# Kernel optimization log

Hardware: AMD Instinct MI355X
Metric: run time of the kernel (lower is better)

The kernel has to match this reference:

```python
import jax, jax.numpy as jnp
import numpy as np

PI = 3.1415927410125732
N = 4096
L = 1.28e-3          # box side [m]
VEL = 5e-7
RC = 3.15e-6         # Rc = diameter/2
RR = 8e-6
RO = 2.5e-5
RA = np.inf
DT_TRANS = 1.4e-14   # DT (translational diffusion)
DR = 0.0028
GAMMA = 25.0
DT = 0.2             # timestep dt
COLL_ITERS = 30      # fixed cap for collision-resolution do-while (orig caps at 1000)


def setup_inputs() -> dict:
    key = jax.random.key(0)
    ks = jax.random.split(key, 7)
    pos_re = jax.random.uniform(ks[0], (N,), jnp.float32) * L
    pos_im = jax.random.uniform(ks[1], (N,), jnp.float32) * L
    ang = jax.random.uniform(ks[2], (N,), jnp.float32, -PI, PI)
    ori_re = jnp.cos(ang)
    ori_im = jnp.sin(ang)
    deltas = jax.random.uniform(ks[3], (N,), jnp.float32) * 0.5
    rot_noise = jax.random.normal(ks[4], (N,), jnp.float32)
    tn_re = jax.random.normal(ks[5], (N,), jnp.float32)
    tn_im = jax.random.normal(ks[6], (N,), jnp.float32)
    return {"pos_re": pos_re, "pos_im": pos_im, "ori_re": ori_re, "ori_im": ori_im,
            "deltas": deltas, "rot_noise": rot_noise, "tn_re": tn_re, "tn_im": tn_im}


def _wrap(diff):
    # torch get_anglediff wrap: (-2pi,2pi) -> ~(-pi,pi)
    diff = jnp.where(diff <= -PI, jnp.mod(diff, PI), diff)
    return diff - (diff >= PI).astype(diff.dtype) * (2.0 * PI)


def _anglediff(a, b):
    return _wrap(jnp.angle(a) - jnp.angle(b))


def _cossim(a, b):
    # nn.CosineSimilarity(dim=1, eps=1e-14) on view_as_real vectors
    dot = a.real * b.real + a.imag * b.imag
    na = jnp.maximum(jnp.abs(a), 1e-14)
    nb = jnp.maximum(jnp.abs(b), 1e-14)
    return dot / (na * nb)


def _mvc(W, z):
    # real [n,n] mask @ complex [n] vector
    return W @ z.real + 1j * (W @ z.imag)


def _solve_collisions(pos):
    n = pos.shape[0]
    eye_f = jnp.eye(n, dtype=jnp.float32)
    eye_c = eye_f.astype(pos.dtype)

    def step(p):
        diff = p[None, :] - p[:, None] + eye_c  # [i,j] = pos_j - pos_i; diag dummy 1 (nan-safe)
        absd = jnp.abs(diff)
        coll = absd <= (2.0 * RC - eye_f)       # diag threshold negative -> self excluded
        move = jnp.where(coll, diff / jnp.where(coll, absd, 1.0) * ((2.1 * RC - absd) * 0.5), 0.0)
        return p - move.sum(axis=1), coll.sum()

    def body(carry, _):
        p, cont = carry
        p_new, ncoll = step(p)
        p = jnp.where(cont, p_new, p)           # do-while: apply move, then continue if collisions
        return (p, jnp.logical_and(cont, ncoll > 0)), None

    body = jax.checkpoint(body)
    (pos, _), _ = jax.lax.scan(body, (pos, jnp.array(True)), None, length=COLL_ITERS)
    return pos


def _forward(pos_re, pos_im, ori_re, ori_im, deltas, rot_noise, tn_re, tn_im):
    pos = (pos_re + 1j * pos_im).astype(jnp.complex64)
    ori = (ori_re + 1j * ori_im).astype(jnp.complex64)
    n = pos.shape[0]
    eye_b = jnp.eye(n, dtype=bool)

    # pairwise |pos_i - pos_j|; diag made 1 to keep abs() grad-safe (diag is masked out / re-added below)
    dists = jnp.abs(pos[:, None] - pos[None, :] + jnp.eye(n, dtype=pos.dtype))
    mask_rr = (dists <= RR) & ~eye_b              # repulsion zone, self excluded (eye subtracted in orig)
    mask_ro = (dists <= RO + RC) | eye_b          # orientation zone, self included (diag dist 0 in orig)
    mask_ra = (dists <= RA + RC) | eye_b          # Ra = inf -> all ones

    # alpha == 2*pi exactly -> within_view branch skipped (matches original)
    ang = jnp.angle(ori)
    abs_ad = jnp.abs(_wrap(ang[:, None] - ang[None, :]))
    in_front = abs_ad < PI / 2

    Wrr = (mask_rr & in_front).astype(jnp.float32)
    Wro = mask_ro.astype(jnp.float32)
    Wra = mask_ra.astype(jnp.float32)

    n_r = Wrr.sum(axis=1)
    S = _mvc(Wrr, pos) / jnp.maximum(n_r, 1.0) - pos * jnp.sign(n_r)
    d = -S

    n_a = Wra.sum(axis=1)
    cms = _mvc(Wra, pos) / jnp.maximum(n_a, 1.0)
    Ps = cms - pos * jnp.sign(n_a)

    osum = _mvc(Wro, ori)
    left = Ps * jnp.exp(1j * deltas)
    right = Ps * jnp.exp(-1j * deltas)

    # T (=300) >= T_release (=200): choose best turn by cosine similarity
    best = jnp.where(_cossim(left, osum) >= _cossim(right, osum), left, right)

    has_rep = jnp.abs(d) > 0.0
    d_safe = jnp.where(has_rep, d, jnp.ones_like(d))
    att = jnp.where(has_rep, _anglediff(d_safe, ori), _anglediff(best, ori))

    s2dr = np.float32(np.sqrt(2.0 * DR))
    sdt = np.float32(np.sqrt(DT))
    rot = jnp.exp(1j * (DT * GAMMA * DR * jnp.sin(att) + rot_noise * s2dr * sdt))

    # complex standard normal: real/imag each N(0, 1/sqrt(2))
    tnoise = (tn_re + 1j * tn_im) * np.float32(np.sqrt(0.5)) * np.float32(np.sqrt(2.0 * DT_TRANS))
    trans = DT * VEL * ori + tnoise * sdt

    new_pos = _solve_collisions(pos + trans)
    new_ori = ori * rot

    c2r = lambda z: jnp.stack([z.real, z.imag], axis=-1)
    # [5, N, 2]: positions, orientations, orientation_sums, leftturns, rightturns (real views)
    return jnp.stack([c2r(new_pos), c2r(new_ori), c2r(osum), c2r(left), c2r(right)], axis=0)


def reference(pos_re, pos_im, ori_re, ori_im, deltas, rot_noise, tn_re, tn_im):
    return _forward(pos_re, pos_im, ori_re, ori_im, deltas, rot_noise, tn_re, tn_im)
```

## Files before the change

kernel.cpp:

```cpp
#include <hip/hip_runtime.h>

#define NPART 4096
#define PI_F 3.1415927410125732f
#define TWO_PI_F 6.2831854820251465f
#define NBCAP 14336
#define SENT 4096

__device__ __forceinline__ float wrapf(float d) {
    if (d <= -PI_F) {
        d = fmodf(d, PI_F);
        if (d < 0.0f) d += PI_F;
    }
    if (d >= PI_F) d -= TWO_PI_F;
    return d;
}

__global__ __launch_bounds__(512)
void k_interact(const float* __restrict__ pr, const float* __restrict__ pim,
                const float* __restrict__ orr, const float* __restrict__ oim,
                const float* __restrict__ deltas,
                const float* __restrict__ rot_noise,
                const float* __restrict__ tn_re, const float* __restrict__ tn_im,
                float* __restrict__ out,
                float2* __restrict__ recPos, int* __restrict__ recMeta,
                unsigned short* __restrict__ recNbr, int* __restrict__ gcnt) {
    constexpr float RR_F  = 8e-6f;
    constexpr float RR2   = RR_F * RR_F;
    constexpr float ROC_F = (float)(2.5e-5 + 3.15e-6);
    constexpr float ROC2  = ROC_F * ROC_F;
    constexpr float CUT_F = 14.3e-6f;
    constexpr float CUT2  = CUT_F * CUT_F;

    __shared__ float2 lsP[512];
    __shared__ float2 lsO[512];
    __shared__ float rA0[512], rA1[512], rA2[512], rA3[512], rA4[512];
    __shared__ float rB0[512], rB1[512], rB2[512], rB3[512], rB4[512];
    __shared__ float cr_[512], ci_[512];
    __shared__ int ncnt[16];
    __shared__ unsigned short nbrL[16 * 16];

    int tid = threadIdx.x;
    int li = tid & 7, sl = tid >> 3;
    int i0 = blockIdx.x * 16 + li;
    int i1 = i0 + 8;

    if (tid < 16) ncnt[tid] = 0;

    float pxA = pr[i0], pyA = pim[i0], oxA = orr[i0], oyA = oim[i0];
    float pxB = pr[i1], pyB = pim[i1], oxB = orr[i1], oyB = oim[i1];

    float nAr = 0.0f, SAre = 0.0f, SAim = 0.0f, oAre = 0.0f, oAim = 0.0f;
    float nBr = 0.0f, SBre = 0.0f, SBim = 0.0f, oBre = 0.0f, oBim = 0.0f;
    float cs_re = 0.0f, cs_im = 0.0f;

    for (int c = 0; c < 8; ++c) {
        int j0 = c * 512;
        __syncthreads();
        float jr = pr[j0 + tid], ji = pim[j0 + tid];
        lsP[tid] = make_float2(jr, ji);
        lsO[tid] = make_float2(orr[j0 + tid], oim[j0 + tid]);
        cs_re += jr; cs_im += ji;
        __syncthreads();
#pragma unroll
        for (int t = 0; t < 8; ++t) {
            int jj = sl * 8 + ((t + sl) & 7);
            int j = j0 + jj;
            float2 pv = lsP[jj];
            float drA = pxA - pv.x, diA = pyA - pv.y;
            float d2A = drA * drA + diA * diA;
            float drB = pxB - pv.x, diB = pyB - pv.y;
            float d2B = drB * drB + diB * diB;
            if (__any((d2A <= ROC2) | (d2B <= ROC2))) {
                float2 ov = lsO[jj];
                if (d2A <= ROC2) { oAre += ov.x; oAim += ov.y; }
                float dotA = oxA * ov.x + oyA * ov.y;
                if ((d2A <= RR2) & (dotA > 0.0f) & (j != i0)) {
                    nAr += 1.0f; SAre += pv.x; SAim += pv.y;
                }
                if (d2A <= CUT2 && j != i0) {
                    int slot = atomicAdd(&ncnt[li], 1);
                    if (slot < 16) nbrL[li * 16 + slot] = (unsigned short)j;
                }
                if (d2B <= ROC2) { oBre += ov.x; oBim += ov.y; }
                float dotB = oxB * ov.x + oyB * ov.y;
                if ((d2B <= RR2) & (dotB > 0.0f) & (j != i1)) {
                    nBr += 1.0f; SBre += pv.x; SBim += pv.y;
                }
                if (d2B <= CUT2 && j != i1) {
                    int slot = atomicAdd(&ncnt[li + 8], 1);
                    if (slot < 16) nbrL[(li + 8) * 16 + slot] = (unsigned short)j;
                }
            }
        }
    }

    rA0[tid] = nAr; rA1[tid] = SAre; rA2[tid] = SAim; rA3[tid] = oAre; rA4[tid] = oAim;
    rB0[tid] = nBr; rB1[tid] = SBre; rB2[tid] = SBim; rB3[tid] = oBre; rB4[tid] = oBim;
    cr_[tid] = cs_re; ci_[tid] = cs_im;
    __syncthreads();
    for (int s = 256; s >= 8; s >>= 1) {
        if (tid < s) {
            rA0[tid] += rA0[tid + s]; rA1[tid] += rA1[tid + s];
            rA2[tid] += rA2[tid + s]; rA3[tid] += rA3[tid + s];
            rA4[tid] += rA4[tid + s];
            rB0[tid] += rB0[tid + s]; rB1[tid] += rB1[tid + s];
            rB2[tid] += rB2[tid + s]; rB3[tid] += rB3[tid + s];
            rB4[tid] += rB4[tid + s];
            cr_[tid] += cr_[tid + s];  ci_[tid] += ci_[tid + s];
        }
        __syncthreads();
    }
    if (tid < 4) { cr_[tid] += cr_[tid + 4]; ci_[tid] += ci_[tid + 4]; }
    __syncthreads();
    if (tid < 2) { cr_[tid] += cr_[tid + 2]; ci_[tid] += ci_[tid + 2]; }
    __syncthreads();
    if (tid == 0) { cr_[0] += cr_[1]; ci_[0] += ci_[1]; }
    __syncthreads();

    if (tid < 16) {
        int i = blockIdx.x * 16 + tid;
        float n_r, S_re, S_im, o_re, o_im, px, py, ox, oy;
        if (tid < 8) {
            n_r = rA0[tid]; S_re = rA1[tid]; S_im = rA2[tid];
            o_re = rA3[tid]; o_im = rA4[tid];
            px = pxA; py = pyA; ox = oxA; oy = oyA;
        } else {
            int g = tid - 8;
            n_r = rB0[g]; S_re = rB1[g]; S_im = rB2[g];
            o_re = rB3[g]; o_im = rB4[g];
            px = pxB; py = pyB; ox = oxB; oy = oyB;
        }

        float maxnr = fmaxf(n_r, 1.0f);
        float sgn = (n_r > 0.0f) ? 1.0f : 0.0f;
        float Sre = S_re / maxnr - px * sgn;
        float Sim = S_im / maxnr - py * sgn;
        float d_re = -Sre, d_im = -Sim;

        float cmsx = cr_[0] * (1.0f / 4096.0f);
        float cmsy = ci_[0] * (1.0f / 4096.0f);
        float Ps_re = cmsx - px;
        float Ps_im = cmsy - py;

        float dl = deltas[i];
        float cd = cosf(dl), sd = sinf(dl);
        float l_re = Ps_re * cd - Ps_im * sd;
        float l_im = Ps_re * sd + Ps_im * cd;
        float r_re = Ps_re * cd + Ps_im * sd;
        float r_im = Ps_im * cd - Ps_re * sd;

        float nb   = fmaxf(hypotf(o_re, o_im), 1e-14f);
        float na_l = fmaxf(hypotf(l_re, l_im), 1e-14f);
        float na_r = fmaxf(hypotf(r_re, r_im), 1e-14f);
        float csl = (l_re * o_re + l_im * o_im) / (na_l * nb);
        float csr = (r_re * o_re + r_im * o_im) / (na_r * nb);
        float b_re = (csl >= csr) ? l_re : r_re;
        float b_im = (csl >= csr) ? l_im : r_im;

        float ai = atan2f(oy, ox);
        bool has_rep = (d_re != 0.0f) || (d_im != 0.0f);
        float att;
        if (has_rep) att = wrapf(atan2f(d_im, d_re) - ai);
        else         att = wrapf(atan2f(b_im, b_re) - ai);

        constexpr float GDD  = (float)(0.2 * 25.0 * 0.0028);
        constexpr float S2DR = 0.07483314773547883f;
        constexpr float SDT  = 0.44721359549995793f;
        float theta = GDD * sinf(att) + (rot_noise[i] * S2DR) * SDT;
        float rr_ = cosf(theta), ri_ = sinf(theta);

        float no_re = ox * rr_ - oy * ri_;
        float no_im = ox * ri_ + oy * rr_;

        constexpr float DTVEL = (float)(0.2 * 5e-7);
        constexpr float C1 = 0.70710678118654752f;
        constexpr float C2 = 1.6733200530681511e-07f;
        float t_re = DTVEL * ox + ((tn_re[i] * C1) * C2) * SDT;
        float t_im = DTVEL * oy + ((tn_im[i] * C1) * C2) * SDT;
        float p0x = px + t_re, p0y = py + t_im;

        float2* o2 = (float2*)out;
        o2[i]            = make_float2(p0x, p0y);
        o2[1 * 4096 + i] = make_float2(no_re, no_im);
        o2[2 * 4096 + i] = make_float2(o_re, o_im);
        o2[3 * 4096 + i] = make_float2(l_re, l_im);
        o2[4 * 4096 + i] = make_float2(r_re, r_im);

        int c = min(ncnt[tid], 16);
        if (c > 0) {
            int cp = (c + 3) & ~3;
            int slot = atomicAdd(&gcnt[0], 1);
            int eoff = atomicAdd(&gcnt[1], cp);
            if (eoff + cp <= NBCAP) {
                recPos[slot] = make_float2(p0x, p0y);
                recMeta[slot] = i | (c << 12) | (eoff << 17);
                for (int m = 0; m < cp; ++m)
                    recNbr[eoff + m] = (m < c) ? nbrL[tid * 16 + m]
                                               : (unsigned short)SENT;
            } else {
                recPos[slot] = make_float2(p0x, p0y);
                recMeta[slot] = i;
            }
        }
    }
}

__global__ __launch_bounds__(1024)
void k_coll_all(const float2* __restrict__ recPos, const int* __restrict__ recMeta,
                const unsigned short* __restrict__ recNbr,
                const int* __restrict__ gcnt, float* __restrict__ out) {
    constexpr float TWO_RC  = (float)(2.0 * 3.15e-6);
    constexpr float TWO_RC2 = TWO_RC * TWO_RC;
    constexpr float C21RC   = (float)(2.1 * 3.15e-6);

    __shared__ float2 pos[NPART + 2];
    __shared__ unsigned short stamp[NPART + 2];
    __shared__ int flg[2];

    int tid = threadIdx.x;
    int n = gcnt[0];

    for (int k = tid; k < NPART + 2; k += 1024) stamp[k] = 0xFFFFu;
    if (tid == 0) {
        pos[SENT] = make_float2(1e9f, 1e9f);
        flg[0] = 0; flg[1] = 0;
    }

    float myx[4], myy[4];
    int myi[4], myc[4], myo[4];
    int nq0[4], nq1[4], nq2[4], nq3[4];
    bool mvd[4];
#pragma unroll
    for (int s = 0; s < 4; ++s) {
        int slot = s * 1024 + tid;
        myc[s] = 0; myi[s] = SENT; myo[s] = 0;
        nq0[s] = SENT; nq1[s] = SENT; nq2[s] = SENT; nq3[s] = SENT;
        mvd[s] = false;
        if (slot < n) {
            float2 p = recPos[slot];
            int meta = recMeta[slot];
            myx[s] = p.x; myy[s] = p.y;
            myi[s] = meta & 4095;
            myc[s] = (meta >> 12) & 31;
            myo[s] = (unsigned)meta >> 17;
            pos[myi[s]] = p;
            if (myc[s] > 0) {
                uint2 w = *(const uint2*)&recNbr[myo[s]];
                nq0[s] = w.x & 0xffff; nq1[s] = w.x >> 16;
                nq2[s] = w.y & 0xffff; nq3[s] = w.y >> 16;
            }
        }
    }
    __syncthreads();

    const float2 FARP = make_float2(1e9f, 1e9f);
    for (int it = 0; it < 30; ++it) {
        float nx[4], ny[4];
        int ncs[4];
#pragma unroll
        for (int s = 0; s < 4; ++s) {
            ncs[s] = 0;
            int c = myc[s];
            if (c <= 0) continue;
            bool chk = (it == 0) || mvd[s];
            if (!chk) {
                unsigned last = (unsigned)(it - 1);
                chk = (stamp[nq0[s]] == last);
                if (c > 1) chk |= (stamp[nq1[s]] == last);
                if (c > 2) chk |= (stamp[nq2[s]] == last);
                if (c > 3) chk |= (stamp[nq3[s]] == last);
                for (int m0 = 4; m0 < c && !chk; m0 += 4) {
                    uint2 w = *(const uint2*)&recNbr[myo[s] + m0];
                    chk |= (stamp[w.x & 0xffff] == last);
                    if (m0 + 1 < c) chk |= (stamp[w.x >> 16] == last);
                    if (m0 + 2 < c) chk |= (stamp[w.y & 0xffff] == last);
                    if (m0 + 3 < c) chk |= (stamp[w.y >> 16] == last);
                }
            }
            if (!chk) continue;
            float px = myx[s], py = myy[s];
            float mre = 0.0f, mim = 0.0f;
            int nc = 0;
            float2 q0 = pos[nq0[s]];
            float2 q1 = (c > 1) ? pos[nq1[s]] : FARP;
            float2 q2 = (c > 2) ? pos[nq2[s]] : FARP;
            float2 q3 = (c > 3) ? pos[nq3[s]] : FARP;
#define COLL_ONE(q)                                                     \
            {                                                           \
                float dr = (q).x - px, di = (q).y - py;                 \
                float d2 = dr * dr + di * di;                           \
                if (d2 <= TWO_RC2) {                                    \
                    float a = sqrtf(d2);                                \
                    float mm = (C21RC - a) * 0.5f / a;                  \
                    mre += dr * mm; mim += di * mm; ++nc;               \
                }                                                       \
            }
            COLL_ONE(q0) COLL_ONE(q1) COLL_ONE(q2) COLL_ONE(q3)
            for (int m0 = 4; m0 < c; m0 += 4) {
                uint2 w = *(const uint2*)&recNbr[myo[s] + m0];
                int j0 = w.x & 0xffff, j1 = w.x >> 16;
                int j2 = w.y & 0xffff, j3 = w.y >> 16;
                float2 t0 = pos[j0], t1 = pos[j1], t2 = pos[j2], t3 = pos[j3];
                COLL_ONE(t0) COLL_ONE(t1) COLL_ONE(t2) COLL_ONE(t3)
            }
#undef COLL_ONE
            ncs[s] = nc;
            nx[s] = px - mre; ny[s] = py - mim;
        }
        __syncthreads();
        int any = 0;
#pragma unroll
        for (int s = 0; s < 4; ++s) {
            mvd[s] = (ncs[s] > 0);
            if (ncs[s] > 0) {
                myx[s] = nx[s]; myy[s] = ny[s];
                pos[myi[s]] = make_float2(nx[s], ny[s]);
                stamp[myi[s]] = (unsigned short)it;
                any = 1;
            }
        }
        if (any) flg[it & 1] = 1;
        if (tid == 0) flg[(it + 1) & 1] = 0;
        __syncthreads();
        if (flg[it & 1] == 0) break;
    }

    float2* o2 = (float2*)out;
#pragma unroll
    for (int s = 0; s < 4; ++s)
        if (s * 1024 + tid < n) o2[myi[s]] = make_float2(myx[s], myy[s]);
}

extern "C" void kernel_launch(void* const* d_in, const int* in_sizes, int n_in,
                              void* d_out, int out_size, void* d_ws, size_t ws_size,
                              hipStream_t stream) {
    const float* pos_re = (const float*)d_in[0];
    const float* pos_im = (const float*)d_in[1];
    const float* ori_re = (const float*)d_in[2];
    const float* ori_im = (const float*)d_in[3];
    const float* deltas = (const float*)d_in[4];
    const float* rot_noise = (const float*)d_in[5];
    const float* tn_re = (const float*)d_in[6];
    const float* tn_im = (const float*)d_in[7];
    float* out = (float*)d_out;

    int* gcnt = (int*)d_ws;
    float2* recPos = (float2*)((char*)d_ws + 16);
    int* recMeta   = (int*)(recPos + NPART);
    unsigned short* recNbr = (unsigned short*)(recMeta + NPART);

    hipMemsetAsync(gcnt, 0, 16, stream);
    k_interact<<<256, 512, 0, stream>>>(pos_re, pos_im, ori_re, ori_im,
                                        deltas, rot_noise, tn_re, tn_im,
                                        out, recPos, recMeta, recNbr, gcnt);
    k_coll_all<<<1, 1024, 0, stream>>>(recPos, recMeta, recNbr, gcnt, out);
}
```

Baseline: 124.2 us.

## Use fixed-slot neighbor lists and push-style dirty flags in collision solver

Replaces the atomic-compacted record list with a fixed 16-slot neighbor array indexed directly by particle id, which removes the global atomics and the memset launch. The collision kernel now reads positions back from the output buffer. The per-iteration activity check becomes push-based: a particle that moved stamps all its neighbors, so the pull-side check is a single flag lookup instead of a scan over neighbor stamps. In exchange, writes scatter into shared flags, which relies on neighbor lists being symmetric, and there are more idle threads because each particle keeps a fixed slot.

Measured after the change: 117.5 us. 5.4% less time.

```diff
diff --git a/kernel.cpp b/kernel.cpp
--- a/kernel.cpp
+++ b/kernel.cpp
@@ -3,7 +3,6 @@
 #define NPART 4096
 #define PI_F 3.1415927410125732f
 #define TWO_PI_F 6.2831854820251465f
-#define NBCAP 14336
 #define SENT 4096
 
 __device__ __forceinline__ float wrapf(float d) {
@@ -22,8 +21,7 @@
                 const float* __restrict__ rot_noise,
                 const float* __restrict__ tn_re, const float* __restrict__ tn_im,
                 float* __restrict__ out,
-                float2* __restrict__ recPos, int* __restrict__ recMeta,
-                unsigned short* __restrict__ recNbr, int* __restrict__ gcnt) {
+                int* __restrict__ recMeta, unsigned short* __restrict__ recNbr) {
     constexpr float RR_F  = 8e-6f;
     constexpr float RR2   = RR_F * RR_F;
     constexpr float ROC_F = (float)(2.5e-5 + 3.15e-6);
@@ -187,68 +185,52 @@
         o2[4 * 4096 + i] = make_float2(r_re, r_im);
 
         int c = min(ncnt[tid], 16);
-        if (c > 0) {
-            int cp = (c + 3) & ~3;
-            int slot = atomicAdd(&gcnt[0], 1);
-            int eoff = atomicAdd(&gcnt[1], cp);
-            if (eoff + cp <= NBCAP) {
-                recPos[slot] = make_float2(p0x, p0y);
-                recMeta[slot] = i | (c << 12) | (eoff << 17);
-                for (int m = 0; m < cp; ++m)
-                    recNbr[eoff + m] = (m < c) ? nbrL[tid * 16 + m]
-                                               : (unsigned short)SENT;
-            } else {
-                recPos[slot] = make_float2(p0x, p0y);
-                recMeta[slot] = i;
-            }
-        }
+        recMeta[i] = c;
+        for (int m = 0; m < c; ++m) recNbr[i * 16 + m] = nbrL[tid * 16 + m];
     }
 }
 
 __global__ __launch_bounds__(1024)
-void k_coll_all(const float2* __restrict__ recPos, const int* __restrict__ recMeta,
+void k_coll_all(const int* __restrict__ recMeta,
                 const unsigned short* __restrict__ recNbr,
-                const int* __restrict__ gcnt, float* __restrict__ out) {
+                float* __restrict__ out) {
     constexpr float TWO_RC  = (float)(2.0 * 3.15e-6);
     constexpr float TWO_RC2 = TWO_RC * TWO_RC;
     constexpr float C21RC   = (float)(2.1 * 3.15e-6);
 
     __shared__ float2 pos[NPART + 2];
-    __shared__ unsigned short stamp[NPART + 2];
+    __shared__ unsigned short ntf[NPART + 2];
     __shared__ int flg[2];
 
     int tid = threadIdx.x;
-    int n = gcnt[0];
-
-    for (int k = tid; k < NPART + 2; k += 1024) stamp[k] = 0xFFFFu;
+    float2* o2 = (float2*)out;
+
+    for (int k = tid; k < NPART + 2; k += 1024) ntf[k] = 0xFFFFu;
     if (tid == 0) {
         pos[SENT] = make_float2(1e9f, 1e9f);
         flg[0] = 0; flg[1] = 0;
     }
 
     float myx[4], myy[4];
-    int myi[4], myc[4], myo[4];
+    int myc[4];
     int nq0[4], nq1[4], nq2[4], nq3[4];
     bool mvd[4];
 #pragma unroll
     for (int s = 0; s < 4; ++s) {
-        int slot = s * 1024 + tid;
-        myc[s] = 0; myi[s] = SENT; myo[s] = 0;
+        int i = s * 1024 + tid;
+        int c = recMeta[i];
+        myc[s] = c;
         nq0[s] = SENT; nq1[s] = SENT; nq2[s] = SENT; nq3[s] = SENT;
         mvd[s] = false;
-        if (slot < n) {
-            float2 p = recPos[slot];
-            int meta = recMeta[slot];
+        if (c > 0) {
+            float2 p = o2[i];
             myx[s] = p.x; myy[s] = p.y;
-            myi[s] = meta & 4095;
-            myc[s] = (meta >> 12) & 31;
-            myo[s] = (unsigned)meta >> 17;
-            pos[myi[s]] = p;
-            if (myc[s] > 0) {
-                uint2 w = *(const uint2*)&recNbr[myo[s]];
-                nq0[s] = w.x & 0xffff; nq1[s] = w.x >> 16;
-                nq2[s] = w.y & 0xffff; nq3[s] = w.y >> 16;
-            }
+            pos[i] = p;
+            uint2 w = *(const uint2*)&recNbr[i * 16];
+            nq0[s] = (int)(w.x & 0xffff);
+            if (c > 1) nq1[s] = (int)(w.x >> 16);
+            if (c > 2) nq2[s] = (int)(w.y & 0xffff);
+            if (c > 3) nq3[s] = (int)(w.y >> 16);
         }
     }
     __syncthreads();
@@ -257,26 +239,14 @@
     for (int it = 0; it < 30; ++it) {
         float nx[4], ny[4];
         int ncs[4];
+        unsigned short last = (unsigned short)(it - 1);
 #pragma unroll
         for (int s = 0; s < 4; ++s) {
             ncs[s] = 0;
             int c = myc[s];
             if (c <= 0) continue;
-            bool chk = (it == 0) || mvd[s];
-            if (!chk) {
-                unsigned last = (unsigned)(it - 1);
-                chk = (stamp[nq0[s]] == last);
-                if (c > 1) chk |= (stamp[nq1[s]] == last);
-                if (c > 2) chk |= (stamp[nq2[s]] == last);
-                if (c > 3) chk |= (stamp[nq3[s]] == last);
-                for (int m0 = 4; m0 < c && !chk; m0 += 4) {
-                    uint2 w = *(const uint2*)&recNbr[myo[s] + m0];
-                    chk |= (stamp[w.x & 0xffff] == last);
-                    if (m0 + 1 < c) chk |= (stamp[w.x >> 16] == last);
-                    if (m0 + 2 < c) chk |= (stamp[w.y & 0xffff] == last);
-                    if (m0 + 3 < c) chk |= (stamp[w.y >> 16] == last);
-                }
-            }
+            int i = s * 1024 + tid;
+            bool chk = (it == 0) || mvd[s] || (ntf[i] == last);
             if (!chk) continue;
             float px = myx[s], py = myy[s];
             float mre = 0.0f, mim = 0.0f;
@@ -297,9 +267,11 @@
             }
             COLL_ONE(q0) COLL_ONE(q1) COLL_ONE(q2) COLL_ONE(q3)
             for (int m0 = 4; m0 < c; m0 += 4) {
-                uint2 w = *(const uint2*)&recNbr[myo[s] + m0];
-                int j0 = w.x & 0xffff, j1 = w.x >> 16;
-                int j2 = w.y & 0xffff, j3 = w.y >> 16;
+                uint2 w = *(const uint2*)&recNbr[i * 16 + m0];
+                int j0 = (int)(w.x & 0xffff);
+                int j1 = (m0 + 1 < c) ? (int)(w.x >> 16) : SENT;
+                int j2 = (m0 + 2 < c) ? (int)(w.y & 0xffff) : SENT;
+                int j3 = (m0 + 3 < c) ? (int)(w.y >> 16) : SENT;
                 float2 t0 = pos[j0], t1 = pos[j1], t2 = pos[j2], t3 = pos[j3];
                 COLL_ONE(t0) COLL_ONE(t1) COLL_ONE(t2) COLL_ONE(t3)
             }
@@ -309,13 +281,26 @@
         }
         __syncthreads();
         int any = 0;
+        unsigned short cur = (unsigned short)it;
 #pragma unroll
         for (int s = 0; s < 4; ++s) {
             mvd[s] = (ncs[s] > 0);
             if (ncs[s] > 0) {
+                int i = s * 1024 + tid;
+                int c = myc[s];
                 myx[s] = nx[s]; myy[s] = ny[s];
-                pos[myi[s]] = make_float2(nx[s], ny[s]);
-                stamp[myi[s]] = (unsigned short)it;
+                pos[i] = make_float2(nx[s], ny[s]);
+                ntf[nq0[s]] = cur;
+                if (c > 1) ntf[nq1[s]] = cur;
+                if (c > 2) ntf[nq2[s]] = cur;
+                if (c > 3) ntf[nq3[s]] = cur;
+                for (int m0 = 4; m0 < c; m0 += 4) {
+                    uint2 w = *(const uint2*)&recNbr[i * 16 + m0];
+                    ntf[w.x & 0xffff] = cur;
+                    if (m0 + 1 < c) ntf[w.x >> 16] = cur;
+                    if (m0 + 2 < c) ntf[w.y & 0xffff] = cur;
+                    if (m0 + 3 < c) ntf[w.y >> 16] = cur;
+                }
                 any = 1;
             }
         }
@@ -325,10 +310,11 @@
         if (flg[it & 1] == 0) break;
     }
 
-    float2* o2 = (float2*)out;
-#pragma unroll
-    for (int s = 0; s < 4; ++s)
-        if (s * 1024 + tid < n) o2[myi[s]] = make_float2(myx[s], myy[s]);
+#pragma unroll
+    for (int s = 0; s < 4; ++s) {
+        int i = s * 1024 + tid;
+        if (myc[s] > 0) o2[i] = make_float2(myx[s], myy[s]);
+    }
 }
 
 extern "C" void kernel_launch(void* const* d_in, const int* in_sizes, int n_in,
@@ -344,14 +330,11 @@
     const float* tn_im = (const float*)d_in[7];
     float* out = (float*)d_out;
 
-    int* gcnt = (int*)d_ws;
-    float2* recPos = (float2*)((char*)d_ws + 16);
-    int* recMeta   = (int*)(recPos + NPART);
+    int* recMeta = (int*)d_ws;
     unsigned short* recNbr = (unsigned short*)(recMeta + NPART);
 
-    hipMemsetAsync(gcnt, 0, 16, stream);
     k_interact<<<256, 512, 0, stream>>>(pos_re, pos_im, ori_re, ori_im,
                                         deltas, rot_noise, tn_re, tn_im,
-                                        out, recPos, recMeta, recNbr, gcnt);
-    k_coll_all<<<1, 1024, 0, stream>>>(recPos, recMeta, recNbr, gcnt, out);
+                                        out, recMeta, recNbr);
+    k_coll_all<<<1, 1024, 0, stream>>>(recMeta, recNbr, out);
 }
```
